# Kernel optimization log

Measured on AMD Instinct MI355X. Metric: run time of the kernel, lower is better.

The kernel has to match this reference:

```python
import jax, jax.numpy as jnp
import numpy as np

B, IN, E, H, MO, OUT, K = 32768, 512, 8, 128, 256, 2, 2


def setup_inputs() -> dict:
    key = jax.random.key(0)
    ks = jax.random.split(key, 9)
    g = lambda k, shape, fan: (jax.random.normal(k, shape, jnp.float32) / np.sqrt(fan)).astype(jnp.float32)
    return {
        "num_prop": jax.random.normal(ks[0], (B, IN), jnp.float32),
        "cat_prop": jax.random.normal(ks[1], (B, 3), jnp.float32),
        "w_gate": g(ks[2], (IN, E), IN),
        "W1": g(ks[3], (E, IN, H), IN),
        "b1": jnp.zeros((E, H), jnp.float32),
        "W2": g(ks[4], (E, H, MO), H),
        "b2": jnp.zeros((E, MO), jnp.float32),
        "Wout": g(ks[5], (MO, OUT), MO),
        "bout": jnp.zeros((OUT,), jnp.float32),
    }


def _cv_squared(v):
    # torch.var is unbiased (ddof=1); eps = 1e-10
    return jnp.var(v, ddof=1) / (jnp.mean(v) ** 2 + 1e-10)


def reference(num_prop, cat_prop, w_gate, W1, b1, W2, b2, Wout, bout):
    b = num_prop.shape[0]
    x = num_prop  # eval mode: dropout is identity, gating noise disabled
    # --- top-k gating ---
    logits = x @ w_gate                                   # [B, E]
    top_vals, top_idx = jax.lax.top_k(logits, K)          # [B, K]
    gate_vals = jax.nn.softmax(top_vals, axis=-1)         # softmax over top-k logits
    gates = jnp.zeros_like(logits).at[jnp.arange(b)[:, None], top_idx].add(gate_vals)  # [B, E]
    # --- load-balancing loss ---
    importance = gates.sum(axis=0)                        # [E]
    load = (gates > 0).astype(jnp.float32).sum(axis=0)    # [E]
    loss = (_cv_squared(importance) + _cv_squared(load)) * 1e-2
    # --- experts (dense-equivalent: gates zero out non-selected experts) ---
    h = jax.nn.relu(jnp.einsum('bi,eih->beh', x, W1) + b1)          # [B, E, H]
    eo = jax.nn.softmax(jnp.einsum('beh,ehm->bem', h, W2) + b2, axis=-1)  # [B, E, MO]
    y = jnp.einsum('be,bem->bm', gates, eo)               # [B, MO]
    # --- output head ---
    out = y @ Wout + bout                                 # [B, OUT]
    return out, loss
```

## Files before the change

kernel.cpp:

```cpp
#include <hip/hip_runtime.h>

#define BN 32768
#define IN 512
#define NE 8
#define NH 128
#define MO 256

typedef const __attribute__((address_space(1))) unsigned int gu32;
typedef __attribute__((address_space(3))) unsigned int lu32;
typedef __attribute__((ext_vector_type(8))) short bf16x8;
typedef __attribute__((ext_vector_type(4))) float f32x4;

__device__ __forceinline__ void cp16(const float* g, float* l) {
    __builtin_amdgcn_global_load_lds((gu32*)g, (lu32*)l, 16, 0, 0);
}

__device__ __forceinline__ unsigned short f2bf(float f) {
    unsigned int u = __float_as_uint(f);
    u = (u + 0x7fffu + ((u >> 16) & 1u)) >> 16;
    return (unsigned short)u;
}
__device__ __forceinline__ float bf2f(unsigned short h) {
    return __uint_as_float((unsigned int)h << 16);
}

__global__ __launch_bounds__(256) void gate_kernel(
    const float* __restrict__ x, const float* __restrict__ wg,
    int* __restrict__ gcount, int* __restrict__ gload, float* __restrict__ gimp,
    int* __restrict__ idx_list, float* __restrict__ gate_list,
    float* __restrict__ out, const float* __restrict__ bout)
{
    __shared__ __align__(16) char wb[32768];
    __shared__ int counts_s[NE];
    __shared__ int load_s[NE];
    __shared__ float imp_s[NE];
    __shared__ int base_s[NE];
    __shared__ int rec_e[128];
    __shared__ int rec_p[128];
    __shared__ float rec_g[128];

    int tid = threadIdx.x;
    if (tid < NE) { counts_s[tid] = 0; load_s[tid] = 0; imp_s[tid] = 0.f; }
    if (tid < 128) {
        int row = blockIdx.x * 64 + (tid >> 1);
        out[row * 2 + (tid & 1)] = bout[tid & 1];
    }
    for (int idx = tid; idx < 1024; idx += 256) {
        int ks = idx >> 6, ls = idx & 63;
        int col = ls & 15;
        int kb = 32 * ks + 8 * (ls >> 4);
        unsigned int ph[4], pl[4];
        #pragma unroll
        for (int j = 0; j < 4; ++j) {
            float v0 = (col < 8) ? wg[(kb + 2 * j) * NE + col] : 0.f;
            float v1 = (col < 8) ? wg[(kb + 2 * j + 1) * NE + col] : 0.f;
            unsigned short h0 = f2bf(v0), h1 = f2bf(v1);
            unsigned short l0 = f2bf(v0 - bf2f(h0)), l1 = f2bf(v1 - bf2f(h1));
            ph[j] = (unsigned int)h0 | ((unsigned int)h1 << 16);
            pl[j] = (unsigned int)l0 | ((unsigned int)l1 << 16);
        }
        *(int4*)(wb + ks * 1024 + ls * 16) = make_int4(ph[0], ph[1], ph[2], ph[3]);
        *(int4*)(wb + 16384 + ks * 1024 + ls * 16) = make_int4(pl[0], pl[1], pl[2], pl[3]);
    }
    __syncthreads();

    int w = tid >> 6, l = tid & 63;
    int e = l & 15;
    int rowA = blockIdx.x * 64 + w * 16 + e;
    const float* px = x + (size_t)rowA * IN + 8 * (l >> 4);

    f32x4 acc = {};
    #pragma unroll
    for (int ks = 0; ks < 16; ++ks) {
        float4 qa = *(const float4*)(px + 32 * ks);
        float4 qb = *(const float4*)(px + 32 * ks + 4);
        float v[8] = {qa.x, qa.y, qa.z, qa.w, qb.x, qb.y, qb.z, qb.w};
        bf16x8 ah, al;
        #pragma unroll
        for (int i = 0; i < 8; ++i) {
            unsigned short h = f2bf(v[i]);
            ah[i] = (short)h;
            al[i] = (short)f2bf(v[i] - bf2f(h));
        }
        bf16x8 bh = *(const bf16x8*)(wb + ks * 1024 + l * 16);
        bf16x8 bl = *(const bf16x8*)(wb + 16384 + ks * 1024 + l * 16);
        acc = __builtin_amdgcn_mfma_f32_16x16x32_bf16(ah, bh, acc, 0, 0, 0);
        acc = __builtin_amdgcn_mfma_f32_16x16x32_bf16(ah, bl, acc, 0, 0, 0);
        acc = __builtin_amdgcn_mfma_f32_16x16x32_bf16(al, bh, acc, 0, 0, 0);
    }

    #pragma unroll
    for (int reg = 0; reg < 4; ++reg) {
        int rloc = w * 16 + 4 * (l >> 4) + reg;
        int row = blockIdx.x * 64 + rloc;
        float lv = (e < 8) ? acc[reg] : -1e30f;

        float v0 = lv; int e0 = e;
        #pragma unroll
        for (int m = 1; m < 8; m <<= 1) {
            float vo = __shfl_xor(v0, m, 64);
            int eo = __shfl_xor(e0, m, 64);
            if (vo > v0 || (vo == v0 && eo < e0)) { v0 = vo; e0 = eo; }
        }
        float v1 = (e == e0 || e >= 8) ? -1e30f : lv; int e1 = e;
        #pragma unroll
        for (int m = 1; m < 8; m <<= 1) {
            float vo = __shfl_xor(v1, m, 64);
            int eo = __shfl_xor(e1, m, 64);
            if (vo > v1 || (vo == v1 && eo < e1)) { v1 = vo; e1 = eo; }
        }
        float v2 = (e == e0 || e == e1 || e >= 8) ? -1e30f : lv;
        #pragma unroll
        for (int m = 1; m < 8; m <<= 1) v2 = fmaxf(v2, __shfl_xor(v2, m, 64));

        double dv0 = v0, dv1 = v1;
        int f0 = e0, f1 = e1;
        if (e < 8 && v1 - v2 < 2e-4f) {
            const float* xr = x + (size_t)row * IN;
            double d0 = 0, d1 = 0, d2 = 0, d3 = 0;
            for (int k = 0; k < IN; k += 4) {
                float4 xv = *(const float4*)(xr + k);
                d0 = fma((double)xv.x, (double)wg[(k    ) * NE + e], d0);
                d1 = fma((double)xv.y, (double)wg[(k + 1) * NE + e], d1);
                d2 = fma((double)xv.z, (double)wg[(k + 2) * NE + e], d2);
                d3 = fma((double)xv.w, (double)wg[(k + 3) * NE + e], d3);
            }
            double ad = (d0 + d1) + (d2 + d3);
            double w0 = ad; int g0i = e;
            #pragma unroll
            for (int m = 1; m < 8; m <<= 1) {
                double vo = __shfl_xor(w0, m, 64);
                int eo = __shfl_xor(g0i, m, 64);
                if (vo > w0 || (vo == w0 && eo < g0i)) { w0 = vo; g0i = eo; }
            }
            double w1 = (e == g0i) ? -1.0e300 : ad; int g1i = e;
            #pragma unroll
            for (int m = 1; m < 8; m <<= 1) {
                double vo = __shfl_xor(w1, m, 64);
                int eo = __shfl_xor(g1i, m, 64);
                if (vo > w1 || (vo == w1 && eo < g1i)) { w1 = vo; g1i = eo; }
            }
            dv0 = w0; dv1 = w1; f0 = g0i; f1 = g1i;
        }

        if (e == 0) {
            float t1 = expf((float)(dv1 - dv0));
            float s = 1.f + t1;
            float g0 = 1.f / s;
            float g1 = t1 / s;
            atomicAdd(&imp_s[f0], g0);
            atomicAdd(&imp_s[f1], g1);
            if (g0 > 0.f) atomicAdd(&load_s[f0], 1);
            if (g1 > 0.f) atomicAdd(&load_s[f1], 1);
            int p0 = atomicAdd(&counts_s[f0], 1);
            int p1 = atomicAdd(&counts_s[f1], 1);
            int rl = rloc * 2;
            rec_e[rl] = f0; rec_e[rl + 1] = f1;
            rec_g[rl] = g0; rec_g[rl + 1] = g1;
            rec_p[rl] = p0; rec_p[rl + 1] = p1;
        }
    }
    __syncthreads();
    if (tid < NE) {
        base_s[tid] = atomicAdd(&gcount[tid], counts_s[tid]);
        atomicAdd(&gimp[tid], imp_s[tid]);
        atomicAdd(&gload[tid], load_s[tid]);
    }
    __syncthreads();
    if (tid < 128) {
        int ee = rec_e[tid];
        int pos = base_s[ee] + rec_p[tid];
        int rw = blockIdx.x * 64 + (tid >> 1);
        idx_list[ee * BN + pos] = rw;
        gate_list[ee * BN + pos] = rec_g[tid];
    }
}

__global__ __launch_bounds__(256) void prep_kernel(
    const float* __restrict__ W1, const float* __restrict__ W2,
    float* __restrict__ W1F, float* __restrict__ W2F)
{
    __shared__ __align__(16) char pb[32768];
    int t = threadIdx.x, b = blockIdx.x;
    if (b < 64) {
        int e = b >> 3, kt = b & 7;
        const float* src = W1 + ((size_t)e * IN + kt * 64) * NH;
        #pragma unroll
        for (int p = 0; p < 8; ++p) {
            int li = p * 256 + t;
            float4 q = *(const float4*)(src + li * 4);
            int kl = li >> 5, n0 = (li & 31) * 4;
            int ks = kl >> 5, g = (kl >> 3) & 3, kb = (kl & 7) * 2;
            float vv[4] = {q.x, q.y, q.z, q.w};
            #pragma unroll
            for (int j = 0; j < 4; ++j) {
                int n = n0 + j;
                int off = (((ks * 8 + (n >> 4)) * 64) + (n & 15) + 16 * g) * 16 + kb;
                unsigned short hh = f2bf(vv[j]);
                unsigned short hl = f2bf(vv[j] - bf2f(hh));
                *(unsigned short*)(pb + off) = hh;
                *(unsigned short*)(pb + 16384 + off) = hl;
            }
        }
        __syncthreads();
        float* dst = W1F + (size_t)b * 8192;
        #pragma unroll
        for (int p = 0; p < 8; ++p) {
            int li = p * 256 + t;
            *(int4*)(dst + li * 4) = *(const int4*)(pb + li * 16);
        }
    } else if (b < 96) {
        int bi = b - 64;
        int e = bi >> 2, kt = bi & 3;
        const float* src = W2 + ((size_t)e * NH + kt * 32) * MO;
        #pragma unroll
        for (int p = 0; p < 8; ++p) {
            int li = p * 256 + t;
            float4 q = *(const float4*)(src + li * 4);
            int kl = li >> 6, n0 = (li & 63) * 4;
            int g = kl >> 3, kb = (kl & 7) * 2;
            float vv[4] = {q.x, q.y, q.z, q.w};
            #pragma unroll
            for (int j = 0; j < 4; ++j) {
                int n = n0 + j;
                int off = ((n >> 4) * 64 + (n & 15) + 16 * g) * 16 + kb;
                unsigned short hh = f2bf(vv[j]);
                unsigned short hl = f2bf(vv[j] - bf2f(hh));
                *(unsigned short*)(pb + off) = hh;
                *(unsigned short*)(pb + 16384 + off) = hl;
            }
        }
        __syncthreads();
        float* dst = W2F + (size_t)bi * 8192;
        #pragma unroll
        for (int p = 0; p < 8; ++p) {
            int li = p * 256 + t;
            *(int4*)(dst + li * 4) = *(const int4*)(pb + li * 16);
        }
    }
}

#define OFF_AH 0
#define OFF_AL 8192
#define OFF_B1 16384
#define OFF_HH 0
#define OFF_HL 16384
#define OFF_B2 32768

__global__ __launch_bounds__(256, 2) void expert_kernel(
    const float* __restrict__ x,
    const float* __restrict__ b1, const float* __restrict__ b2,
    const float* __restrict__ Wout,
    const float* __restrict__ W1F, const float* __restrict__ W2F,
    const int* __restrict__ gcount,
    const float* __restrict__ gimp, const int* __restrict__ gload,
    const int* __restrict__ idx_list, const float* __restrict__ gate_list,
    float* __restrict__ out)
{
    __shared__ __align__(16) char smx[66560];
    __shared__ float woutS[512];

    int e = blockIdx.y;
    int cnt = gcount[e];
    int row0 = blockIdx.x * 64;
    if (e == 0 && blockIdx.x == 0 && threadIdx.x == 0) {
        float mi = 0.f, ml = 0.f;
        for (int k = 0; k < NE; ++k) { mi += gimp[k]; ml += (float)gload[k]; }
        mi *= 0.125f; ml *= 0.125f;
        float vi = 0.f, vl = 0.f;
        for (int k = 0; k < NE; ++k) {
            float d = gimp[k] - mi;  vi += d * d;
            float d2 = (float)gload[k] - ml; vl += d2 * d2;
        }
        vi *= (1.f / 7.f); vl *= (1.f / 7.f);
        out[BN * 2] = (vi / (mi * mi + 1e-10f) + vl / (ml * ml + 1e-10f)) * 0.01f;
    }
    if (row0 >= cnt) return;
    int t = threadIdx.x;
    int l = t & 63, w = t >> 6;

    woutS[t] = Wout[t];
    woutS[256 + t] = Wout[256 + t];

    int s_mf = t >> 6;
    int s_r  = t & 15;
    int s_g  = (t >> 4) & 3;
    int rloc = s_mf * 16 + s_r;
    int sgi = row0 + rloc; if (sgi >= cnt) sgi = cnt - 1;
    const float* xrow = x + (size_t)idx_list[e * BN + sgi] * IN;

    int mbase = (w & 1) * 2;
    int nsel  = w >> 1;

    f32x4 acc1[2][4] = {};
    for (int kt = 0; kt < 8; ++kt) {
        {
            const float* gb = W1F + (size_t)(e * 8 + kt) * 8192;
            float* lb = (float*)(smx + OFF_B1);
            #pragma unroll
            for (int p = 0; p < 8; ++p)
                cp16(gb + (p * 256 + t) * 4, lb + (p * 256 + t) * 4);
        }
        #pragma unroll
        for (int ks = 0; ks < 2; ++ks) {
            int k = kt * 64 + ks * 32 + s_g * 8;
            float4 qa = *(const float4*)(xrow + k);
            float4 qb = *(const float4*)(xrow + k + 4);
            float vv[8] = {qa.x, qa.y, qa.z, qa.w, qb.x, qb.y, qb.z, qb.w};
            unsigned int dh[4], dl[4];
            #pragma unroll
            for (int j = 0; j < 4; ++j) {
                unsigned short h0 = f2bf(vv[2 * j]);
                unsigned short h1 = f2bf(vv[2 * j + 1]);
                unsigned short l0 = f2bf(vv[2 * j] - bf2f(h0));
                unsigned short l1 = f2bf(vv[2 * j + 1] - bf2f(h1));
                dh[j] = (unsigned int)h0 | ((unsigned int)h1 << 16);
                dl[j] = (unsigned int)l0 | ((unsigned int)l1 << 16);
            }
            int slot = ((ks * 4 + s_mf) * 64 + (s_r + 16 * s_g)) * 16;
            *(int4*)(smx + OFF_AH + slot) = make_int4(dh[0], dh[1], dh[2], dh[3]);
            *(int4*)(smx + OFF_AL + slot) = make_int4(dl[0], dl[1], dl[2], dl[3]);
        }
        __syncthreads();
        #pragma unroll
        for (int ks = 0; ks < 2; ++ks) {
            bf16x8 ah[2], al[2];
            #pragma unroll
            for (int mf = 0; mf < 2; ++mf) {
                int ao = ((ks * 4 + mbase + mf) * 64 + l) * 16;
                ah[mf] = *(const bf16x8*)(smx + OFF_AH + ao);
                al[mf] = *(const bf16x8*)(smx + OFF_AL + ao);
            }
            #pragma unroll
            for (int nf = 0; nf < 4; ++nf) {
                int bo = ((ks * 8 + nsel * 4 + nf) * 64 + l) * 16;
                bf16x8 bh = *(const bf16x8*)(smx + OFF_B1 + bo);
                bf16x8 bl = *(const bf16x8*)(smx + OFF_B1 + 16384 + bo);
                #pragma unroll
                for (int mf = 0; mf < 2; ++mf) {
                    acc1[mf][nf] = __builtin_amdgcn_mfma_f32_16x16x32_bf16(ah[mf], bh, acc1[mf][nf], 0, 0, 0);
                    acc1[mf][nf] = __builtin_amdgcn_mfma_f32_16x16x32_bf16(ah[mf], bl, acc1[mf][nf], 0, 0, 0);
                    acc1[mf][nf] = __builtin_amdgcn_mfma_f32_16x16x32_bf16(al[mf], bh, acc1[mf][nf], 0, 0, 0);
                    acc1[mf][nf] = __builtin_amdgcn_mfma_f32_16x16x32_bf16(al[mf], bl, acc1[mf][nf], 0, 0, 0);
                }
            }
        }
        __syncthreads();
    }

    #pragma unroll
    for (int mf = 0; mf < 2; ++mf) {
        int mf2 = (w & 1) * 2 + mf;
        int rlow = 4 * (l >> 4);
        #pragma unroll
        for (int nf = 0; nf < 4; ++nf) {
            int c = nsel * 64 + nf * 16 + (l & 15);
            float b1v = b1[e * NH + c];
            int ks2 = c >> 5;
            int g2 = (c >> 3) & 3;
            int boff = ((ks2 * 4 + mf2) * 64) * 16 + (c & 7) * 2;
            #pragma unroll
            for (int rg = 0; rg < 4; ++rg) {
                float v = fmaxf(acc1[mf][nf][rg] + b1v, 0.f);
                unsigned short hh = f2bf(v);
                unsigned short hl = f2bf(v - bf2f(hh));
                int off = boff + ((rlow + rg) + 16 * g2) * 16;
                *(unsigned short*)(smx + OFF_HH + off) = hh;
                *(unsigned short*)(smx + OFF_HL + off) = hl;
            }
        }
    }
    __syncthreads();

    f32x4 acc2[2][8] = {};
    for (int kt2 = 0; kt2 < 4; ++kt2) {
        {
            const float* gb = W2F + (size_t)(e * 4 + kt2) * 8192;
            float* lb = (float*)(smx + OFF_B2);
            #pragma unroll
            for (int p = 0; p < 8; ++p)
                cp16(gb + (p * 256 + t) * 4, lb + (p * 256 + t) * 4);
        }
        __syncthreads();
        bf16x8 ah[2], al[2];
        #pragma unroll
        for (int mf = 0; mf < 2; ++mf) {
            int ao = ((kt2 * 4 + (w & 1) * 2 + mf) * 64 + l) * 16;
            ah[mf] = *(const bf16x8*)(smx + OFF_HH + ao);
            al[mf] = *(const bf16x8*)(smx + OFF_HL + ao);
        }
        #pragma unroll
        for (int nf = 0; nf < 8; ++nf) {
            int bo = ((nsel * 8 + nf) * 64 + l) * 16;
            bf16x8 bh = *(const bf16x8*)(smx + OFF_B2 + bo);
            bf16x8 bl = *(const bf16x8*)(smx + OFF_B2 + 16384 + bo);
            #pragma unroll
            for (int mf = 0; mf < 2; ++mf) {
                acc2[mf][nf] = __builtin_amdgcn_mfma_f32_16x16x32_bf16(ah[mf], bh, acc2[mf][nf], 0, 0, 0);
                acc2[mf][nf] = __builtin_amdgcn_mfma_f32_16x16x32_bf16(ah[mf], bl, acc2[mf][nf], 0, 0, 0);
                acc2[mf][nf] = __builtin_amdgcn_mfma_f32_16x16x32_bf16(al[mf], bh, acc2[mf][nf], 0, 0, 0);
                acc2[mf][nf] = __builtin_amdgcn_mfma_f32_16x16x32_bf16(al[mf], bl, acc2[mf][nf], 0, 0, 0);
            }
        }
        __syncthreads();
    }

    float* zl = (float*)smx;
    #pragma unroll
    for (int mf = 0; mf < 2; ++mf) {
        int rbase = (w & 1) * 32 + mf * 16 + 4 * (l >> 4);
        #pragma unroll
        for (int nf = 0; nf < 8; ++nf) {
            int c = nsel * 128 + nf * 16 + (l & 15);
            float b2v = b2[e * MO + c];
            #pragma unroll
            for (int rg = 0; rg < 4; ++rg)
                zl[(rbase + rg) * 260 + c] = acc2[mf][nf][rg] + b2v;
        }
    }
    __syncthreads();

    int rr = w * 16 + (l >> 2);
    int c0 = l & 3;
    float vreg[64];
    float m = -1e30f;
    #pragma unroll
    for (int j = 0; j < 64; ++j) {
        vreg[j] = zl[rr * 260 + c0 + 4 * j];
        m = fmaxf(m, vreg[j]);
    }
    m = fmaxf(m, __shfl_xor(m, 1, 64));
    m = fmaxf(m, __shfl_xor(m, 2, 64));
    float s = 0.f, o0 = 0.f, o1 = 0.f;
    #pragma unroll
    for (int j = 0; j < 64; ++j) {
        float tt = __expf(vreg[j] - m);
        s += tt;
        float2 wv = *(const float2*)&woutS[(c0 + 4 * j) * 2];
        o0 = fmaf(tt, wv.x, o0);
        o1 = fmaf(tt, wv.y, o1);
    }
    s  += __shfl_xor(s, 1, 64);  s  += __shfl_xor(s, 2, 64);
    o0 += __shfl_xor(o0, 1, 64); o0 += __shfl_xor(o0, 2, 64);
    o1 += __shfl_xor(o1, 1, 64); o1 += __shfl_xor(o1, 2, 64);
    if (c0 == 0) {
        int gi = row0 + rr;
        if (gi < cnt) {
            float g = gate_list[e * BN + gi];
            int brow = idx_list[e * BN + gi];
            float inv = 1.f / s;
            atomicAdd(&out[brow * 2 + 0], g * o0 * inv);
            atomicAdd(&out[brow * 2 + 1], g * o1 * inv);
        }
    }
}

extern "C" void kernel_launch(void* const* d_in, const int* in_sizes, int n_in,
                              void* d_out, int out_size, void* d_ws, size_t ws_size,
                              hipStream_t stream) {
    const float* x    = (const float*)d_in[0];
    const float* wg   = (const float*)d_in[2];
    const float* W1   = (const float*)d_in[3];
    const float* b1   = (const float*)d_in[4];
    const float* W2   = (const float*)d_in[5];
    const float* b2   = (const float*)d_in[6];
    const float* Wout = (const float*)d_in[7];
    const float* bout = (const float*)d_in[8];
    float* out = (float*)d_out;

    char* ws = (char*)d_ws;
    int*   gcount    = (int*)(ws + 0);
    int*   gload     = (int*)(ws + 32);
    float* gimp      = (float*)(ws + 64);
    int*   idx_list  = (int*)(ws + 128);
    float* gate_list = (float*)(ws + 128 + sizeof(int) * NE * BN);
    float* W1F       = (float*)(ws + 128 + 8 * NE * BN);
    float* W2F       = (float*)(ws + 128 + 8 * NE * BN + 64 * 32768);

    hipMemsetAsync(ws, 0, 128, stream);
    prep_kernel<<<96, 256, 0, stream>>>(W1, W2, W1F, W2F);
    gate_kernel<<<BN / 64, 256, 0, stream>>>(x, wg, gcount, gload, gimp,
                                             idx_list, gate_list, out, bout);
    dim3 eg(BN / 64, NE);
    expert_kernel<<<eg, 256, 0, stream>>>(x, b1, b2, Wout, W1F, W2F,
                                          gcount, gimp, gload,
                                          idx_list, gate_list, out);
}
```

Baseline: 216.6 us.

## Merge weight prep into gate kernel and restructure expert warp tiling for occupancy

Folds the weight-repacking blocks into the gate kernel as extra blocks, removing one kernel launch. The expert kernel switches each warp to own a full 16-row slice across all columns, which removes duplicated A-fragment work. W2 tiles are streamed in smaller halves, so LDS drops from about 65KB to 48KB and launch bounds rise to 3 blocks per CU. The softmax and output head now run directly from accumulator registers with cross-lane shuffles instead of going through an LDS round-trip. The risks are higher register pressure from 16 accumulators and extra barriers during the W2 streaming.

```diff
diff --git a/kernel.cpp b/kernel.cpp
--- a/kernel.cpp
+++ b/kernel.cpp
@@ -24,8 +24,10 @@
     return __uint_as_float((unsigned int)h << 16);
 }
 
-__global__ __launch_bounds__(256) void gate_kernel(
+__global__ __launch_bounds__(256) void gatep_kernel(
     const float* __restrict__ x, const float* __restrict__ wg,
+    const float* __restrict__ W1, const float* __restrict__ W2,
+    float* __restrict__ W1F, float* __restrict__ W2F,
     int* __restrict__ gcount, int* __restrict__ gload, float* __restrict__ gimp,
     int* __restrict__ idx_list, float* __restrict__ gate_list,
     float* __restrict__ out, const float* __restrict__ bout)
@@ -40,9 +42,73 @@
     __shared__ float rec_g[128];
 
     int tid = threadIdx.x;
+    int bx = blockIdx.x;
+
+    if (bx >= 512) {
+        char* pb = wb;
+        int t = tid, b = bx - 512;
+        if (b < 64) {
+            int e = b >> 3, kt = b & 7;
+            const float* src = W1 + ((size_t)e * IN + kt * 64) * NH;
+            #pragma unroll
+            for (int p = 0; p < 8; ++p) {
+                int li = p * 256 + t;
+                float4 q = *(const float4*)(src + li * 4);
+                int kl = li >> 5, n0 = (li & 31) * 4;
+                int ks = kl >> 5, g = (kl >> 3) & 3, kb = (kl & 7) * 2;
+                float vv[4] = {q.x, q.y, q.z, q.w};
+                #pragma unroll
+                for (int j = 0; j < 4; ++j) {
+                    int n = n0 + j;
+                    int off = (((ks * 8 + (n >> 4)) * 64) + (n & 15) + 16 * g) * 16 + kb;
+                    unsigned short hh = f2bf(vv[j]);
+                    unsigned short hl = f2bf(vv[j] - bf2f(hh));
+                    *(unsigned short*)(pb + off) = hh;
+                    *(unsigned short*)(pb + 16384 + off) = hl;
+                }
+            }
+            __syncthreads();
+            float* dst = W1F + (size_t)b * 8192;
+            #pragma unroll
+            for (int p = 0; p < 8; ++p) {
+                int li = p * 256 + t;
+                *(int4*)(dst + li * 4) = *(const int4*)(pb + li * 16);
+            }
+        } else {
+            int bi = b - 64;
+            int e = bi >> 2, kt = bi & 3;
+            const float* src = W2 + ((size_t)e * NH + kt * 32) * MO;
+            #pragma unroll
+            for (int p = 0; p < 8; ++p) {
+                int li = p * 256 + t;
+                float4 q = *(const float4*)(src + li * 4);
+                int kl = li >> 6, n0 = (li & 63) * 4;
+                int g = kl >> 3, kb = (kl & 7) * 2;
+                float vv[4] = {q.x, q.y, q.z, q.w};
+                #pragma unroll
+                for (int j = 0; j < 4; ++j) {
+                    int n = n0 + j;
+                    int off = ((n >> 4) * 64 + (n & 15) + 16 * g) * 16 + kb;
+                    unsigned short hh = f2bf(vv[j]);
+                    unsigned short hl = f2bf(vv[j] - bf2f(hh));
+                    *(unsigned short*)(pb + off) = hh;
+                    *(unsigned short*)(pb + 16384 + off) = hl;
+                }
+            }
+            __syncthreads();
+            float* dst = W2F + (size_t)bi * 8192;
+            #pragma unroll
+            for (int p = 0; p < 8; ++p) {
+                int li = p * 256 + t;
+                *(int4*)(dst + li * 4) = *(const int4*)(pb + li * 16);
+            }
+        }
+        return;
+    }
+
     if (tid < NE) { counts_s[tid] = 0; load_s[tid] = 0; imp_s[tid] = 0.f; }
     if (tid < 128) {
-        int row = blockIdx.x * 64 + (tid >> 1);
+        int row = bx * 64 + (tid >> 1);
         out[row * 2 + (tid & 1)] = bout[tid & 1];
     }
     for (int idx = tid; idx < 1024; idx += 256) {
@@ -66,7 +132,7 @@
 
     int w = tid >> 6, l = tid & 63;
     int e = l & 15;
-    int rowA = blockIdx.x * 64 + w * 16 + e;
+    int rowA = bx * 64 + w * 16 + e;
     const float* px = x + (size_t)rowA * IN + 8 * (l >> 4);
 
     f32x4 acc = {};
@@ -92,7 +158,7 @@
     #pragma unroll
     for (int reg = 0; reg < 4; ++reg) {
         int rloc = w * 16 + 4 * (l >> 4) + reg;
-        int row = blockIdx.x * 64 + rloc;
+        int row = bx * 64 + rloc;
         float lv = (e < 8) ? acc[reg] : -1e30f;
 
         float v0 = lv; int e0 = e;
@@ -170,84 +236,13 @@
     if (tid < 128) {
         int ee = rec_e[tid];
         int pos = base_s[ee] + rec_p[tid];
-        int rw = blockIdx.x * 64 + (tid >> 1);
+        int rw = bx * 64 + (tid >> 1);
         idx_list[ee * BN + pos] = rw;
         gate_list[ee * BN + pos] = rec_g[tid];
     }
 }
 
-__global__ __launch_bounds__(256) void prep_kernel(
-    const float* __restrict__ W1, const float* __restrict__ W2,
-    float* __restrict__ W1F, float* __restrict__ W2F)
-{
-    __shared__ __align__(16) char pb[32768];
-    int t = threadIdx.x, b = blockIdx.x;
-    if (b < 64) {
-        int e = b >> 3, kt = b & 7;
-        const float* src = W1 + ((size_t)e * IN + kt * 64) * NH;
-        #pragma unroll
-        for (int p = 0; p < 8; ++p) {
-            int li = p * 256 + t;
-            float4 q = *(const float4*)(src + li * 4);
-            int kl = li >> 5, n0 = (li & 31) * 4;
-            int ks = kl >> 5, g = (kl >> 3) & 3, kb = (kl & 7) * 2;
-            float vv[4] = {q.x, q.y, q.z, q.w};
-            #pragma unroll
-            for (int j = 0; j < 4; ++j) {
-                int n = n0 + j;
-                int off = (((ks * 8 + (n >> 4)) * 64) + (n & 15) + 16 * g) * 16 + kb;
-                unsigned short hh = f2bf(vv[j]);
-                unsigned short hl = f2bf(vv[j] - bf2f(hh));
-                *(unsigned short*)(pb + off) = hh;
-                *(unsigned short*)(pb + 16384 + off) = hl;
-            }
-        }
-        __syncthreads();
-        float* dst = W1F + (size_t)b * 8192;
-        #pragma unroll
-        for (int p = 0; p < 8; ++p) {
-            int li = p * 256 + t;
-            *(int4*)(dst + li * 4) = *(const int4*)(pb + li * 16);
-        }
-    } else if (b < 96) {
-        int bi = b - 64;
-        int e = bi >> 2, kt = bi & 3;
-        const float* src = W2 + ((size_t)e * NH + kt * 32) * MO;
-        #pragma unroll
-        for (int p = 0; p < 8; ++p) {
-            int li = p * 256 + t;
-            float4 q = *(const float4*)(src + li * 4);
-            int kl = li >> 6, n0 = (li & 63) * 4;
-            int g = kl >> 3, kb = (kl & 7) * 2;
-            float vv[4] = {q.x, q.y, q.z, q.w};
-            #pragma unroll
-            for (int j = 0; j < 4; ++j) {
-                int n = n0 + j;
-                int off = ((n >> 4) * 64 + (n & 15) + 16 * g) * 16 + kb;
-                unsigned short hh = f2bf(vv[j]);
-                unsigned short hl = f2bf(vv[j] - bf2f(hh));
-                *(unsigned short*)(pb + off) = hh;
-                *(unsigned short*)(pb + 16384 + off) = hl;
-            }
-        }
-        __syncthreads();
-        float* dst = W2F + (size_t)bi * 8192;
-        #pragma unroll
-        for (int p = 0; p < 8; ++p) {
-            int li = p * 256 + t;
-            *(int4*)(dst + li * 4) = *(const int4*)(pb + li * 16);
-        }
-    }
-}
-
-#define OFF_AH 0
-#define OFF_AL 8192
-#define OFF_B1 16384
-#define OFF_HH 0
-#define OFF_HL 16384
-#define OFF_B2 32768
-
-__global__ __launch_bounds__(256, 2) void expert_kernel(
+__global__ __launch_bounds__(256, 3) void expert_kernel(
     const float* __restrict__ x,
     const float* __restrict__ b1, const float* __restrict__ b2,
     const float* __restrict__ Wout,
@@ -257,7 +252,7 @@
     const int* __restrict__ idx_list, const float* __restrict__ gate_list,
     float* __restrict__ out)
 {
-    __shared__ __align__(16) char smx[66560];
+    __shared__ __align__(16) char smx[49152];
     __shared__ float woutS[512];
 
     int e = blockIdx.y;
@@ -282,21 +277,21 @@
     woutS[t] = Wout[t];
     woutS[256 + t] = Wout[256 + t];
 
-    int s_mf = t >> 6;
     int s_r  = t & 15;
     int s_g  = (t >> 4) & 3;
-    int rloc = s_mf * 16 + s_r;
-    int sgi = row0 + rloc; if (sgi >= cnt) sgi = cnt - 1;
+    int s_mf = t >> 6;
+    int rloc_s = s_mf * 16 + s_r;
+    int sgi = row0 + rloc_s; if (sgi >= cnt) sgi = cnt - 1;
     const float* xrow = x + (size_t)idx_list[e * BN + sgi] * IN;
 
-    int mbase = (w & 1) * 2;
-    int nsel  = w >> 1;
-
-    f32x4 acc1[2][4] = {};
+    const float* W1e = W1F + (size_t)e * 65536;
+    const float* W2e = W2F + (size_t)e * 32768;
+
+    f32x4 acc1[8] = {};
     for (int kt = 0; kt < 8; ++kt) {
         {
-            const float* gb = W1F + (size_t)(e * 8 + kt) * 8192;
-            float* lb = (float*)(smx + OFF_B1);
+            const float* gb = W1e + (size_t)kt * 8192;
+            float* lb = (float*)(smx + 16384);
             #pragma unroll
             for (int p = 0; p < 8; ++p)
                 cp16(gb + (p * 256 + t) * 4, lb + (p * 256 + t) * 4);
@@ -318,139 +313,123 @@
                 dl[j] = (unsigned int)l0 | ((unsigned int)l1 << 16);
             }
             int slot = ((ks * 4 + s_mf) * 64 + (s_r + 16 * s_g)) * 16;
-            *(int4*)(smx + OFF_AH + slot) = make_int4(dh[0], dh[1], dh[2], dh[3]);
-            *(int4*)(smx + OFF_AL + slot) = make_int4(dl[0], dl[1], dl[2], dl[3]);
+            *(int4*)(smx + slot) = make_int4(dh[0], dh[1], dh[2], dh[3]);
+            *(int4*)(smx + 8192 + slot) = make_int4(dl[0], dl[1], dl[2], dl[3]);
         }
         __syncthreads();
         #pragma unroll
         for (int ks = 0; ks < 2; ++ks) {
-            bf16x8 ah[2], al[2];
-            #pragma unroll
-            for (int mf = 0; mf < 2; ++mf) {
-                int ao = ((ks * 4 + mbase + mf) * 64 + l) * 16;
-                ah[mf] = *(const bf16x8*)(smx + OFF_AH + ao);
-                al[mf] = *(const bf16x8*)(smx + OFF_AL + ao);
-            }
-            #pragma unroll
-            for (int nf = 0; nf < 4; ++nf) {
-                int bo = ((ks * 8 + nsel * 4 + nf) * 64 + l) * 16;
-                bf16x8 bh = *(const bf16x8*)(smx + OFF_B1 + bo);
-                bf16x8 bl = *(const bf16x8*)(smx + OFF_B1 + 16384 + bo);
-                #pragma unroll
-                for (int mf = 0; mf < 2; ++mf) {
-                    acc1[mf][nf] = __builtin_amdgcn_mfma_f32_16x16x32_bf16(ah[mf], bh, acc1[mf][nf], 0, 0, 0);
-                    acc1[mf][nf] = __builtin_amdgcn_mfma_f32_16x16x32_bf16(ah[mf], bl, acc1[mf][nf], 0, 0, 0);
-                    acc1[mf][nf] = __builtin_amdgcn_mfma_f32_16x16x32_bf16(al[mf], bh, acc1[mf][nf], 0, 0, 0);
-                    acc1[mf][nf] = __builtin_amdgcn_mfma_f32_16x16x32_bf16(al[mf], bl, acc1[mf][nf], 0, 0, 0);
-                }
+            int ao = ((ks * 4 + w) * 64 + l) * 16;
+            bf16x8 ah = *(const bf16x8*)(smx + ao);
+            bf16x8 al = *(const bf16x8*)(smx + 8192 + ao);
+            #pragma unroll
+            for (int nf = 0; nf < 8; ++nf) {
+                int bo = ((ks * 8 + nf) * 64 + l) * 16;
+                bf16x8 bh = *(const bf16x8*)(smx + 16384 + bo);
+                bf16x8 bl = *(const bf16x8*)(smx + 32768 + bo);
+                acc1[nf] = __builtin_amdgcn_mfma_f32_16x16x32_bf16(ah, bh, acc1[nf], 0, 0, 0);
+                acc1[nf] = __builtin_amdgcn_mfma_f32_16x16x32_bf16(ah, bl, acc1[nf], 0, 0, 0);
+                acc1[nf] = __builtin_amdgcn_mfma_f32_16x16x32_bf16(al, bh, acc1[nf], 0, 0, 0);
+                acc1[nf] = __builtin_amdgcn_mfma_f32_16x16x32_bf16(al, bl, acc1[nf], 0, 0, 0);
             }
         }
         __syncthreads();
     }
 
-    #pragma unroll
-    for (int mf = 0; mf < 2; ++mf) {
-        int mf2 = (w & 1) * 2 + mf;
+    {
         int rlow = 4 * (l >> 4);
         #pragma unroll
-        for (int nf = 0; nf < 4; ++nf) {
-            int c = nsel * 64 + nf * 16 + (l & 15);
+        for (int nf = 0; nf < 8; ++nf) {
+            int c = nf * 16 + (l & 15);
             float b1v = b1[e * NH + c];
-            int ks2 = c >> 5;
+            int kt2c = c >> 5;
             int g2 = (c >> 3) & 3;
-            int boff = ((ks2 * 4 + mf2) * 64) * 16 + (c & 7) * 2;
+            int boff = ((kt2c * 4 + w) * 64) * 16 + (c & 7) * 2;
             #pragma unroll
             for (int rg = 0; rg < 4; ++rg) {
-                float v = fmaxf(acc1[mf][nf][rg] + b1v, 0.f);
+                float v = fmaxf(acc1[nf][rg] + b1v, 0.f);
                 unsigned short hh = f2bf(v);
                 unsigned short hl = f2bf(v - bf2f(hh));
                 int off = boff + ((rlow + rg) + 16 * g2) * 16;
-                *(unsigned short*)(smx + OFF_HH + off) = hh;
-                *(unsigned short*)(smx + OFF_HL + off) = hl;
+                *(unsigned short*)(smx + off) = hh;
+                *(unsigned short*)(smx + 16384 + off) = hl;
             }
         }
     }
     __syncthreads();
 
-    f32x4 acc2[2][8] = {};
+    f32x4 acc2[16] = {};
     for (int kt2 = 0; kt2 < 4; ++kt2) {
-        {
-            const float* gb = W2F + (size_t)(e * 4 + kt2) * 8192;
-            float* lb = (float*)(smx + OFF_B2);
-            #pragma unroll
-            for (int p = 0; p < 8; ++p)
-                cp16(gb + (p * 256 + t) * 4, lb + (p * 256 + t) * 4);
-        }
-        __syncthreads();
-        bf16x8 ah[2], al[2];
-        #pragma unroll
-        for (int mf = 0; mf < 2; ++mf) {
-            int ao = ((kt2 * 4 + (w & 1) * 2 + mf) * 64 + l) * 16;
-            ah[mf] = *(const bf16x8*)(smx + OFF_HH + ao);
-            al[mf] = *(const bf16x8*)(smx + OFF_HL + ao);
-        }
-        #pragma unroll
-        for (int nf = 0; nf < 8; ++nf) {
-            int bo = ((nsel * 8 + nf) * 64 + l) * 16;
-            bf16x8 bh = *(const bf16x8*)(smx + OFF_B2 + bo);
-            bf16x8 bl = *(const bf16x8*)(smx + OFF_B2 + 16384 + bo);
-            #pragma unroll
-            for (int mf = 0; mf < 2; ++mf) {
-                acc2[mf][nf] = __builtin_amdgcn_mfma_f32_16x16x32_bf16(ah[mf], bh, acc2[mf][nf], 0, 0, 0);
-                acc2[mf][nf] = __builtin_amdgcn_mfma_f32_16x16x32_bf16(ah[mf], bl, acc2[mf][nf], 0, 0, 0);
-                acc2[mf][nf] = __builtin_amdgcn_mfma_f32_16x16x32_bf16(al[mf], bh, acc2[mf][nf], 0, 0, 0);
-                acc2[mf][nf] = __builtin_amdgcn_mfma_f32_16x16x32_bf16(al[mf], bl, acc2[mf][nf], 0, 0, 0);
-            }
-        }
-        __syncthreads();
-    }
-
-    float* zl = (float*)smx;
+        int ao = ((kt2 * 4 + w) * 64 + l) * 16;
+        bf16x8 ah2 = *(const bf16x8*)(smx + ao);
+        bf16x8 al2 = *(const bf16x8*)(smx + 16384 + ao);
+        #pragma unroll
+        for (int nh2 = 0; nh2 < 2; ++nh2) {
+            {
+                const float* gh = W2e + kt2 * 8192 + nh2 * 2048;
+                const float* gl = W2e + kt2 * 8192 + 4096 + nh2 * 2048;
+                float* lb = (float*)(smx + 32768);
+                #pragma unroll
+                for (int p = 0; p < 2; ++p) {
+                    cp16(gh + (p * 256 + t) * 4, lb + (p * 256 + t) * 4);
+                    cp16(gl + (p * 256 + t) * 4, lb + 2048 + (p * 256 + t) * 4);
+                }
+            }
+            __syncthreads();
+            #pragma unroll
+            for (int nf2 = 0; nf2 < 8; ++nf2) {
+                int bo = (nf2 * 64 + l) * 16;
+                bf16x8 bh = *(const bf16x8*)(smx + 32768 + bo);
+                bf16x8 bl = *(const bf16x8*)(smx + 40960 + bo);
+                int nf = nh2 * 8 + nf2;
+                acc2[nf] = __builtin_amdgcn_mfma_f32_16x16x32_bf16(ah2, bh, acc2[nf], 0, 0, 0);
+                acc2[nf] = __builtin_amdgcn_mfma_f32_16x16x32_bf16(ah2, bl, acc2[nf], 0, 0, 0);
+                acc2[nf] = __builtin_amdgcn_mfma_f32_16x16x32_bf16(al2, bh, acc2[nf], 0, 0, 0);
+                acc2[nf] = __builtin_amdgcn_mfma_f32_16x16x32_bf16(al2, bl, acc2[nf], 0, 0, 0);
+            }
+            __syncthreads();
+        }
+    }
+
     #pragma unroll
-    for (int mf = 0; mf < 2; ++mf) {
-        int rbase = (w & 1) * 32 + mf * 16 + 4 * (l >> 4);
-        #pragma unroll
-        for (int nf = 0; nf < 8; ++nf) {
-            int c = nsel * 128 + nf * 16 + (l & 15);
-            float b2v = b2[e * MO + c];
-            #pragma unroll
-            for (int rg = 0; rg < 4; ++rg)
-                zl[(rbase + rg) * 260 + c] = acc2[mf][nf][rg] + b2v;
-        }
-    }
-    __syncthreads();
-
-    int rr = w * 16 + (l >> 2);
-    int c0 = l & 3;
-    float vreg[64];
-    float m = -1e30f;
+    for (int nf = 0; nf < 16; ++nf) {
+        float b2v = b2[e * MO + nf * 16 + (l & 15)];
+        #pragma unroll
+        for (int rg = 0; rg < 4; ++rg) acc2[nf][rg] += b2v;
+    }
     #pragma unroll
-    for (int j = 0; j < 64; ++j) {
-        vreg[j] = zl[rr * 260 + c0 + 4 * j];
-        m = fmaxf(m, vreg[j]);
-    }
-    m = fmaxf(m, __shfl_xor(m, 1, 64));
-    m = fmaxf(m, __shfl_xor(m, 2, 64));
-    float s = 0.f, o0 = 0.f, o1 = 0.f;
-    #pragma unroll
-    for (int j = 0; j < 64; ++j) {
-        float tt = __expf(vreg[j] - m);
-        s += tt;
-        float2 wv = *(const float2*)&woutS[(c0 + 4 * j) * 2];
-        o0 = fmaf(tt, wv.x, o0);
-        o1 = fmaf(tt, wv.y, o1);
-    }
-    s  += __shfl_xor(s, 1, 64);  s  += __shfl_xor(s, 2, 64);
-    o0 += __shfl_xor(o0, 1, 64); o0 += __shfl_xor(o0, 2, 64);
-    o1 += __shfl_xor(o1, 1, 64); o1 += __shfl_xor(o1, 2, 64);
-    if (c0 == 0) {
-        int gi = row0 + rr;
-        if (gi < cnt) {
-            float g = gate_list[e * BN + gi];
-            int brow = idx_list[e * BN + gi];
-            float inv = 1.f / s;
-            atomicAdd(&out[brow * 2 + 0], g * o0 * inv);
-            atomicAdd(&out[brow * 2 + 1], g * o1 * inv);
+    for (int rg = 0; rg < 4; ++rg) {
+        float m = -1e30f;
+        #pragma unroll
+        for (int nf = 0; nf < 16; ++nf) m = fmaxf(m, acc2[nf][rg]);
+        m = fmaxf(m, __shfl_xor(m, 1, 64));
+        m = fmaxf(m, __shfl_xor(m, 2, 64));
+        m = fmaxf(m, __shfl_xor(m, 4, 64));
+        m = fmaxf(m, __shfl_xor(m, 8, 64));
+        float s = 0.f, o0 = 0.f, o1 = 0.f;
+        #pragma unroll
+        for (int nf = 0; nf < 16; ++nf) {
+            float tt = __expf(acc2[nf][rg] - m);
+            s += tt;
+            float2 wv = *(const float2*)&woutS[2 * (nf * 16 + (l & 15))];
+            o0 = fmaf(tt, wv.x, o0);
+            o1 = fmaf(tt, wv.y, o1);
+        }
+        s += __shfl_xor(s, 1, 64); s += __shfl_xor(s, 2, 64);
+        s += __shfl_xor(s, 4, 64); s += __shfl_xor(s, 8, 64);
+        o0 += __shfl_xor(o0, 1, 64); o0 += __shfl_xor(o0, 2, 64);
+        o0 += __shfl_xor(o0, 4, 64); o0 += __shfl_xor(o0, 8, 64);
+        o1 += __shfl_xor(o1, 1, 64); o1 += __shfl_xor(o1, 2, 64);
+        o1 += __shfl_xor(o1, 4, 64); o1 += __shfl_xor(o1, 8, 64);
+        if ((l & 15) == 0) {
+            int gi = row0 + w * 16 + 4 * (l >> 4) + rg;
+            if (gi < cnt) {
+                float g = gate_list[e * BN + gi];
+                int brow = idx_list[e * BN + gi];
+                float inv = 1.f / s;
+                atomicAdd(&out[brow * 2 + 0], g * o0 * inv);
+                atomicAdd(&out[brow * 2 + 1], g * o1 * inv);
+            }
         }
     }
 }
@@ -478,9 +457,9 @@
     float* W2F       = (float*)(ws + 128 + 8 * NE * BN + 64 * 32768);
 
     hipMemsetAsync(ws, 0, 128, stream);
-    prep_kernel<<<96, 256, 0, stream>>>(W1, W2, W1F, W2F);
-    gate_kernel<<<BN / 64, 256, 0, stream>>>(x, wg, gcount, gload, gimp,
-                                             idx_list, gate_list, out, bout);
+    gatep_kernel<<<608, 256, 0, stream>>>(x, wg, W1, W2, W1F, W2F,
+                                          gcount, gload, gimp,
+                                          idx_list, gate_list, out, bout);
     dim3 eg(BN / 64, NE);
     expert_kernel<<<eg, 256, 0, stream>>>(x, b1, b2, Wout, W1F, W2F,
                                           gcount, gimp, gload,
```

Result: faster. 209.0 us (-3.5%).
